# Kernel tuning notes

Hardware: AMD Instinct MI355X
Metric: run time of the kernel (lower is better)

## Reference

```python
import jax, jax.numpy as jnp
import numpy as np

NUM_SLOTS = 8
SLOT_DIM = 3
WRITE_RATE = 0.1


def _amu(x, memory, Wk, bk, Ww, bw, Wg, bg, Wo, bo):
    """Associative Memory Unit.
    x: [B, T, Din], memory: [B, N, D] -> (outputs [B, T, Dout], memory [B, N, D]).
    Per step: softmax key-addressing read, gated erase/add write at WRITE_RATE,
    output = Linear(concat(x_t, read)).
    """
    xt = jnp.swapaxes(x, 0, 1)  # [T, B, Din]

    def step(mem, x_t):
        k = x_t @ Wk + bk                                   # [B, D]
        scores = jnp.einsum('bnd,bd->bn', mem, k)           # [B, N]
        w = jax.nn.softmax(scores, axis=-1)                 # addressing weights
        read = jnp.einsum('bn,bnd->bd', w, mem)             # [B, D]
        v = x_t @ Ww + bw                                   # write vector [B, D]
        e = jax.nn.sigmoid(x_t @ Wg + bg)                   # erase gate [B, D]
        we = w[:, :, None] * e[:, None, :]                  # [B, N, D]
        mem = mem * (1.0 - WRITE_RATE * we) + WRITE_RATE * w[:, :, None] * v[:, None, :]
        out = jnp.concatenate([x_t, read], axis=-1) @ Wo + bo
        return mem, out

    mem, outs = jax.lax.scan(step, memory, xt)
    return jnp.swapaxes(outs, 0, 1), mem


def setup_inputs() -> dict:
    key = jax.random.key(0)
    ks = jax.random.split(key, 12)
    B, T, D_in, D_hid, D_out = 64, 512, 128, 512, 128
    s = 0.05
    return {
        'inp': jax.random.normal(ks[0], (B, T, D_in), jnp.float32),
        'W1k': jax.random.normal(ks[1], (D_in, SLOT_DIM), jnp.float32) * s,
        'b1k': jnp.zeros((SLOT_DIM,), jnp.float32),
        'W1w': jax.random.normal(ks[2], (D_in, SLOT_DIM), jnp.float32) * s,
        'b1w': jnp.zeros((SLOT_DIM,), jnp.float32),
        'W1g': jax.random.normal(ks[3], (D_in, SLOT_DIM), jnp.float32) * s,
        'b1g': jnp.zeros((SLOT_DIM,), jnp.float32),
        'W1o': jax.random.normal(ks[4], (D_in + SLOT_DIM, D_hid), jnp.float32) * s,
        'b1o': jnp.zeros((D_hid,), jnp.float32),
        'W2k': jax.random.normal(ks[5], (D_hid, SLOT_DIM), jnp.float32) * s,
        'b2k': jnp.zeros((SLOT_DIM,), jnp.float32),
        'W2w': jax.random.normal(ks[6], (D_hid, SLOT_DIM), jnp.float32) * s,
        'b2w': jnp.zeros((SLOT_DIM,), jnp.float32),
        'W2g': jax.random.normal(ks[7], (D_hid, SLOT_DIM), jnp.float32) * s,
        'b2g': jnp.zeros((SLOT_DIM,), jnp.float32),
        'W2o': jax.random.normal(ks[8], (D_hid + SLOT_DIM, D_out), jnp.float32) * s,
        'b2o': jnp.zeros((D_out,), jnp.float32),
    }


def reference(inp, W1k, b1k, W1w, b1w, W1g, b1g, W1o, b1o,
              W2k, b2k, W2w, b2w, W2g, b2g, W2o, b2o):
    B = inp.shape[0]
    mem0 = jnp.zeros((B, NUM_SLOTS, SLOT_DIM), inp.dtype)
    o1, mem = _amu(inp, mem0, W1k, b1k, W1w, b1w, W1g, b1g, W1o, b1o)
    o1 = jax.nn.sigmoid(o1)  # self.layers = Sequential(Sigmoid())
    o2, mem = _amu(o1, mem, W2k, b2k, W2w, b2w, W2g, b2g, W2o, b2o)
    out = jax.nn.sigmoid(o2[:, -1, :])  # last timestep, then sigmoid
    return out
```

## Files before the change

kernel.cpp:

```cpp
#include <hip/hip_runtime.h>
#include <hip/hip_bf16.h>

#define B_ 64
#define T_ 512
#define LOG2E 1.4426950408889634f
#define PHASE_STEPS 16
#define NPHASE (T_/PHASE_STEPS)

typedef __attribute__((ext_vector_type(8))) short short8;
typedef __attribute__((ext_vector_type(4))) float f32x4;

__device__ __forceinline__ float fast_exp2(float x){ return __builtin_amdgcn_exp2f(x); }
__device__ __forceinline__ float fast_rcp(float x){ return __builtin_amdgcn_rcpf(x); }
__device__ __forceinline__ float sigmoidf_(float x){ return fast_rcp(1.0f + fast_exp2(-x*LOG2E)); }
__device__ __forceinline__ unsigned short f2bf(float f){
  union{float f; unsigned u;} v; v.f = f;
  unsigned r = v.u + 0x7fffu + ((v.u>>16)&1u);
  return (unsigned short)(r>>16);
}

template<int CTRL>
__device__ __forceinline__ float dpp_xadd(float x){
  int y = __builtin_amdgcn_update_dpp(0, __float_as_int(x), CTRL, 0xf, 0xf, true);
  return x + __int_as_float(y);
}
__device__ __forceinline__ float dpp_sum8(float x){
  x = dpp_xadd<0xB1>(x);
  x = dpp_xadd<0x4E>(x);
  x = dpp_xadd<0x141>(x);
  return x;
}

__global__ __launch_bounds__(256) void k_prep(const float* __restrict__ W1o,
    const float* __restrict__ W2k, const float* __restrict__ W2w, const float* __restrict__ W2g,
    unsigned short* __restrict__ W1oTb, unsigned short* __restrict__ W2cTb)
{
  int idx = blockIdx.x*256 + threadIdx.x;
  if (idx < 65536){
    int n = idx >> 7, k = idx & 127;
    W1oTb[idx] = f2bf(W1o[k*512 + n]);
  }
  if (idx < 8192){
    int j = idx >> 9, c = idx & 511;
    float v = 0.f;
    if (j < 3) v = W2k[c*3 + j];
    else if (j < 6) v = W2w[c*3 + j - 3];
    else if (j < 9) v = W2g[c*3 + j - 6];
    W2cTb[idx] = f2bf(v);
  }
}

__global__ __launch_bounds__(256) void k_proj1(const float* __restrict__ X,
    const float* __restrict__ Wk, const float* __restrict__ bk,
    const float* __restrict__ Ww, const float* __restrict__ bw,
    const float* __restrict__ Wg, const float* __restrict__ bg,
    float* __restrict__ P1)
{
  __shared__ __align__(16) float A[64*132];
  __shared__ float Wc[128*12];
  __shared__ float bb[9];
  int tid = threadIdx.x;
  long r0 = (long)blockIdx.x * 64;
  const float4* X4 = (const float4*)(X + r0*128);
  #pragma unroll
  for (int it=0; it<8; ++it){
    int f4 = tid + it*256;
    float4 v = X4[f4];
    int f = f4*4; int row = f>>7; int k = f&127;
    A[row*132+k]   = v.x; A[row*132+k+1] = v.y;
    A[row*132+k+2] = v.z; A[row*132+k+3] = v.w;
  }
  #pragma unroll
  for (int it=0; it<5; ++it){
    int w = tid + it*256;
    if (w < 1152){
      int k = w/9, j = w%9;
      float val;
      if (j<3) val = Wk[k*3+j]; else if (j<6) val = Ww[k*3+j-3]; else val = Wg[k*3+j-6];
      Wc[k*12+j] = val;
    }
  }
  if (tid < 9){
    float v; if (tid<3) v = bk[tid]; else if (tid<6) v = bw[tid-3]; else v = bg[tid-6];
    bb[tid] = v;
  }
  __syncthreads();
  for (int o = tid; o < 576; o += 256){
    int row = o/9, j = o%9;
    float acc = bb[j];
    #pragma unroll 8
    for (int k=0;k<128;++k) acc = fmaf(A[row*132+k], Wc[k*12+j], acc);
    if (j<3) acc *= LOG2E;
    else if (j<6) acc *= 0.1f;
    else acc = 0.1f * sigmoidf_(acc);
    long r = r0 + row;
    int b = (int)(r >> 9); int t = (int)(r & 511);
    int bh = b >> 5, bl = b & 31;
    P1[((long)bh*512 + t)*288 + j*32 + bl] = acc;
  }
}

template<int STORE_ALL>
__device__ __forceinline__ void scan8(const float* __restrict__ P,
                                      float* __restrict__ Rout, int bh)
{
  __shared__ __align__(16) float buf[2][PHASE_STEPS*288];
  int tid = threadIdx.x;
  int wv = tid >> 6, lane = tid & 63;
  const float* Pb = P + (long)bh*512*288;
  if (wv == 4){
    #pragma unroll 1
    for (int p = 0; p < NPHASE; ++p){
      const float4* src = (const float4*)(Pb + (long)p*PHASE_STEPS*288);
      float4* dst = (float4*)buf[p&1];
      float4 tmp[18];
      #pragma unroll
      for (int i=0;i<18;++i) tmp[i] = src[lane + i*64];
      #pragma unroll
      for (int i=0;i<18;++i) dst[lane + i*64] = tmp[i];
      __syncthreads();
    }
  } else {
    int g = lane >> 3, slot = lane & 7;
    int bl = wv*8 + g;
    int batch = bh*32 + bl;
    float m0=0.f, m1=0.f, m2=0.f;
    __syncthreads();
    #pragma unroll 1
    for (int p = 0; p < NPHASE; ++p){
      const float* bp = buf[p&1];
      float pp[3][9];
      #pragma unroll
      for (int j=0;j<9;++j){ pp[0][j] = bp[j*32+bl]; pp[1][j] = bp[288 + j*32+bl]; }
      #pragma unroll
      for (int s=0;s<PHASE_STEPS;++s){
        if (s+2 < PHASE_STEPS){
          #pragma unroll
          for (int j=0;j<9;++j) pp[(s+2)%3][j] = bp[(s+2)*288 + j*32 + bl];
        }
        const float* pv = pp[s%3];
        float sc = fmaf(m2, pv[2], fmaf(m1, pv[1], m0*pv[0]));
        float pe = fast_exp2(sc);
        float S = dpp_sum8(pe);
        float rinv = fast_rcp(S);
        float w = pe * rinv;
        if (STORE_ALL){
          float r0 = dpp_sum8(pe*m0);
          float r1 = dpp_sum8(pe*m1);
          float r2 = dpp_sum8(pe*m2);
          float rsel = (slot==0) ? r0 : ((slot==1) ? r1 : r2);
          rsel *= rinv;
          if (slot < 3) Rout[((p*PHASE_STEPS+s)*3 + slot)*64 + batch] = rsel;
        } else if (s == PHASE_STEPS-1){
          if (p == NPHASE-1){
            float r0 = dpp_sum8(pe*m0);
            float r1 = dpp_sum8(pe*m1);
            float r2 = dpp_sum8(pe*m2);
            float rsel = (slot==0) ? r0 : ((slot==1) ? r1 : r2);
            rsel *= rinv;
            if (slot < 3) Rout[slot*64 + batch] = rsel;
          }
        }
        float v0=pv[3], v1=pv[4], v2=pv[5], e0=pv[6], e1=pv[7], e2=pv[8];
        m0 = fmaf(w, fmaf(-e0, m0, v0), m0);
        m1 = fmaf(w, fmaf(-e1, m1, v1), m1);
        m2 = fmaf(w, fmaf(-e2, m2, v2), m2);
      }
      if (p < NPHASE-1) __syncthreads();
    }
  }
}

__global__ __launch_bounds__(320) void k_scan1(const float* __restrict__ P1,
                                               float* __restrict__ R1)
{
  scan8<1>(P1, R1, (int)blockIdx.x);
}

__global__ __launch_bounds__(256) void k_fused(const float* __restrict__ X,
    const float* __restrict__ W1o, const float* __restrict__ b1o,
    const float* __restrict__ R1,
    const unsigned short* __restrict__ W1oTb, const unsigned short* __restrict__ W2cTb,
    const float* __restrict__ b2k, const float* __restrict__ b2w, const float* __restrict__ b2g,
    float* __restrict__ P2, float* __restrict__ O1last)
{
  __shared__ __align__(16) float rdS[48];
  __shared__ __align__(16) unsigned short o1b[16*520];
  __shared__ __align__(16) float pSum[4*16*16];
  int tid = threadIdx.x;
  int w = tid >> 6, lane = tid & 63;
  int n16 = lane & 15, g4 = lane >> 4;
  long r0 = (long)blockIdx.x * 16;
  int b = (int)(r0 >> 9); int t0 = (int)(r0 & 511);

  if (tid < 48){
    int i = tid/3, d = tid%3;
    rdS[tid] = R1[((t0+i)*3+d)*64 + b];
  }

  short8 afr[4];
  const float* Xrow = X + (r0 + n16)*128;
  #pragma unroll
  for (int q=0;q<4;++q){
    f32x4 x0 = *(const f32x4*)(Xrow + q*32 + g4*8);
    f32x4 x1 = *(const f32x4*)(Xrow + q*32 + g4*8 + 4);
    short8 a;
    a[0]=(short)f2bf(x0[0]); a[1]=(short)f2bf(x0[1]);
    a[2]=(short)f2bf(x0[2]); a[3]=(short)f2bf(x0[3]);
    a[4]=(short)f2bf(x1[0]); a[5]=(short)f2bf(x1[1]);
    a[6]=(short)f2bf(x1[2]); a[7]=(short)f2bf(x1[3]);
    afr[q]=a;
  }
  __syncthreads();

  f32x4 ra = *(const f32x4*)(rdS + g4*12);
  f32x4 rb = *(const f32x4*)(rdS + g4*12 + 4);
  f32x4 rc = *(const f32x4*)(rdS + g4*12 + 8);
  float rd0[4] = { ra[0], ra[3], rb[2], rc[1] };
  float rd1[4] = { ra[1], rb[0], rb[3], rc[2] };
  float rd2[4] = { ra[2], rb[1], rc[0], rc[3] };

  #pragma unroll
  for (int tt=0; tt<8; ++tt){
    int gc = w*128 + tt*16 + n16;
    f32x4 acc = {0.f,0.f,0.f,0.f};
    #pragma unroll
    for (int q=0;q<4;++q){
      short8 bf = *(const short8*)(W1oTb + gc*128 + q*32 + g4*8);
      acc = __builtin_amdgcn_mfma_f32_16x16x32_bf16(afr[q], bf, acc, 0,0,0);
    }
    float bias = b1o[gc];
    float wr0 = W1o[128*512+gc], wr1 = W1o[129*512+gc], wr2 = W1o[130*512+gc];
    #pragma unroll
    for (int reg=0; reg<4; ++reg){
      int rowloc = g4*4 + reg;
      float z = acc[reg] + bias + rd0[reg]*wr0 + rd1[reg]*wr1 + rd2[reg]*wr2;
      float o1 = sigmoidf_(z);
      o1b[rowloc*520 + gc] = f2bf(o1);
      if (t0 == 496 && rowloc == 15) O1last[b*512 + gc] = o1;
    }
  }

  f32x4 accP = {0.f,0.f,0.f,0.f};
  #pragma unroll
  for (int q2=0; q2<4; ++q2){
    int kk = w*128 + q2*32;
    short8 a2 = *(const short8*)(o1b + n16*520 + kk + g4*8);
    short8 bb2 = *(const short8*)(W2cTb + n16*512 + kk + g4*8);
    accP = __builtin_amdgcn_mfma_f32_16x16x32_bf16(a2, bb2, accP, 0,0,0);
  }
  #pragma unroll
  for (int reg=0;reg<4;++reg){
    int rowloc = g4*4+reg;
    pSum[w*256 + rowloc*16 + n16] = accP[reg];
  }
  __syncthreads();
  if (tid < 144){
    int r = tid/9, j = tid%9;
    float s = pSum[r*16+j] + pSum[256+r*16+j] + pSum[512+r*16+j] + pSum[768+r*16+j];
    float outv;
    if (j<3){ s += b2k[j]; outv = s*LOG2E; }
    else if (j<6){ s += b2w[j-3]; outv = 0.1f*s; }
    else { s += b2g[j-6]; outv = 0.1f*sigmoidf_(s); }
    int t = t0 + r;
    int bh = b >> 5, bl = b & 31;
    P2[((long)bh*512 + t)*288 + j*32 + bl] = outv;
  }
}

__global__ __launch_bounds__(320) void k_scan2_opart(const float* __restrict__ P2,
    float* __restrict__ R2F,
    const float* __restrict__ O1last, const float* __restrict__ W2o,
    const float* __restrict__ b2o, float* __restrict__ Opart)
{
  if (blockIdx.x < 2){
    scan8<0>(P2, R2F, (int)blockIdx.x);
    return;
  }
  __shared__ __align__(16) float s2[512];
  int b = blockIdx.x - 2; int tid = threadIdx.x;
  if (tid < 128)
    ((float4*)s2)[tid] = ((const float4*)(O1last + b*512))[tid];
  __syncthreads();
  if (tid < 128){
    float acc = b2o[tid];
    #pragma unroll 8
    for (int n=0;n<512;++n) acc = fmaf(s2[n], W2o[n*128+tid], acc);
    Opart[b*128+tid] = acc;
  }
}

__global__ __launch_bounds__(256) void k_final(const float* __restrict__ Opart,
    const float* __restrict__ R2F, const float* __restrict__ W2o,
    float* __restrict__ out)
{
  int idx = blockIdx.x*256 + threadIdx.x;
  if (idx < 8192){
    int b = idx >> 7; int o = idx & 127;
    float r0 = R2F[b], r1 = R2F[64+b], r2 = R2F[128+b];
    float v = Opart[idx]
            + r0*W2o[512*128+o] + r1*W2o[513*128+o] + r2*W2o[514*128+o];
    out[idx] = sigmoidf_(v);
  }
}

extern "C" void kernel_launch(void* const* d_in, const int* in_sizes, int n_in,
                              void* d_out, int out_size, void* d_ws, size_t ws_size,
                              hipStream_t stream)
{
  const float* X  = (const float*)d_in[0];
  const float* W1k= (const float*)d_in[1]; const float* b1k=(const float*)d_in[2];
  const float* W1w= (const float*)d_in[3]; const float* b1w=(const float*)d_in[4];
  const float* W1g= (const float*)d_in[5]; const float* b1g=(const float*)d_in[6];
  const float* W1o= (const float*)d_in[7]; const float* b1o=(const float*)d_in[8];
  const float* W2k= (const float*)d_in[9]; const float* b2k=(const float*)d_in[10];
  const float* W2w= (const float*)d_in[11]; const float* b2w=(const float*)d_in[12];
  const float* W2g= (const float*)d_in[13]; const float* b2g=(const float*)d_in[14];
  const float* W2o= (const float*)d_in[15]; const float* b2o=(const float*)d_in[16];

  float* ws = (float*)d_ws;
  float* P1     = ws;
  float* R1     = P1 + 294912;
  float* P2     = R1 + 98304;
  float* O1last = P2 + 294912;
  float* R2F    = O1last + 32768;
  float* Opart  = R2F + 192;
  unsigned short* W1oTb = (unsigned short*)(Opart + 8192);
  unsigned short* W2cTb = W1oTb + 65536;
  float* out    = (float*)d_out;

  hipLaunchKernelGGL(k_prep, dim3(256), dim3(256), 0, stream,
                     W1o, W2k, W2w, W2g, W1oTb, W2cTb);
  hipLaunchKernelGGL(k_proj1, dim3(512), dim3(256), 0, stream,
                     X, W1k,b1k, W1w,b1w, W1g,b1g, P1);
  hipLaunchKernelGGL(k_scan1, dim3(2), dim3(320), 0, stream, P1, R1);
  hipLaunchKernelGGL(k_fused, dim3(2048), dim3(256), 0, stream,
                     X, W1o, b1o, R1, W1oTb, W2cTb, b2k, b2w, b2g, P2, O1last);
  hipLaunchKernelGGL(k_scan2_opart, dim3(66), dim3(320), 0, stream,
                     P2, R2F, O1last, W2o, b2o, Opart);
  hipLaunchKernelGGL(k_final, dim3(32), dim3(256), 0, stream,
                     Opart, R2F, W2o, out);
}
```

Baseline: 261.7 us.

## Slim scan: per-step packed projections, drop LDS staging, defer read reduction

Projection outputs are now stored as 12-float records per (t,batch), so each scan lane loads its step's parameters straight from global memory with register prefetch. This removes the producer wave, LDS double buffering and barriers from the serial scan. Scan1 no longer reduces the read vector per step. It stores the exp weight and memory state per slot, and the fused kernel rebuilds the read vectors with DPP sums. The change also vectorises the proj1 dot products over a transposed weight tile and reuses the P1 buffer for P2. The cost is more global traffic from scan1 and the serial chain waiting on global-load latency.

New measurement: 430.4 us. 64.4% more time.

```diff
diff --git a/kernel.cpp b/kernel.cpp
--- a/kernel.cpp
+++ b/kernel.cpp
@@ -4,8 +4,6 @@
 #define B_ 64
 #define T_ 512
 #define LOG2E 1.4426950408889634f
-#define PHASE_STEPS 16
-#define NPHASE (T_/PHASE_STEPS)
 
 typedef __attribute__((ext_vector_type(8))) short short8;
 typedef __attribute__((ext_vector_type(4))) float f32x4;
@@ -57,7 +55,7 @@
     float* __restrict__ P1)
 {
   __shared__ __align__(16) float A[64*132];
-  __shared__ float Wc[128*12];
+  __shared__ __align__(16) float WcT[9*132];
   __shared__ float bb[9];
   int tid = threadIdx.x;
   long r0 = (long)blockIdx.x * 64;
@@ -67,17 +65,16 @@
     int f4 = tid + it*256;
     float4 v = X4[f4];
     int f = f4*4; int row = f>>7; int k = f&127;
-    A[row*132+k]   = v.x; A[row*132+k+1] = v.y;
-    A[row*132+k+2] = v.z; A[row*132+k+3] = v.w;
+    *(float4*)&A[row*132+k] = v;
   }
   #pragma unroll
   for (int it=0; it<5; ++it){
-    int w = tid + it*256;
-    if (w < 1152){
-      int k = w/9, j = w%9;
+    int w0 = tid + it*256;
+    if (w0 < 1152){
+      int k = w0/9, j = w0%9;
       float val;
       if (j<3) val = Wk[k*3+j]; else if (j<6) val = Ww[k*3+j-3]; else val = Wg[k*3+j-6];
-      Wc[k*12+j] = val;
+      WcT[j*132+k] = val;
     }
   }
   if (tid < 9){
@@ -87,99 +84,88 @@
   __syncthreads();
   for (int o = tid; o < 576; o += 256){
     int row = o/9, j = o%9;
-    float acc = bb[j];
-    #pragma unroll 8
-    for (int k=0;k<128;++k) acc = fmaf(A[row*132+k], Wc[k*12+j], acc);
+    const f32x4* Ar = (const f32x4*)(A + row*132);
+    const f32x4* Wr = (const f32x4*)(WcT + j*132);
+    f32x4 acc4 = {0.f,0.f,0.f,0.f};
+    #pragma unroll
+    for (int k4=0;k4<32;++k4){
+      f32x4 a = Ar[k4], wv = Wr[k4];
+      acc4[0]=fmaf(a[0],wv[0],acc4[0]);
+      acc4[1]=fmaf(a[1],wv[1],acc4[1]);
+      acc4[2]=fmaf(a[2],wv[2],acc4[2]);
+      acc4[3]=fmaf(a[3],wv[3],acc4[3]);
+    }
+    float acc = bb[j] + (acc4[0]+acc4[1]) + (acc4[2]+acc4[3]);
     if (j<3) acc *= LOG2E;
     else if (j<6) acc *= 0.1f;
     else acc = 0.1f * sigmoidf_(acc);
     long r = r0 + row;
     int b = (int)(r >> 9); int t = (int)(r & 511);
-    int bh = b >> 5, bl = b & 31;
-    P1[((long)bh*512 + t)*288 + j*32 + bl] = acc;
-  }
-}
-
-template<int STORE_ALL>
-__device__ __forceinline__ void scan8(const float* __restrict__ P,
-                                      float* __restrict__ Rout, int bh)
-{
-  __shared__ __align__(16) float buf[2][PHASE_STEPS*288];
+    P1[((long)t*64 + b)*12 + j] = acc;
+  }
+}
+
+template<int STORE_SM>
+__device__ __forceinline__ void scan_slim(const float* __restrict__ P,
+                                          float* __restrict__ Out, int bh)
+{
   int tid = threadIdx.x;
-  int wv = tid >> 6, lane = tid & 63;
-  const float* Pb = P + (long)bh*512*288;
-  if (wv == 4){
-    #pragma unroll 1
-    for (int p = 0; p < NPHASE; ++p){
-      const float4* src = (const float4*)(Pb + (long)p*PHASE_STEPS*288);
-      float4* dst = (float4*)buf[p&1];
-      float4 tmp[18];
-      #pragma unroll
-      for (int i=0;i<18;++i) tmp[i] = src[lane + i*64];
-      #pragma unroll
-      for (int i=0;i<18;++i) dst[lane + i*64] = tmp[i];
-      __syncthreads();
-    }
-  } else {
-    int g = lane >> 3, slot = lane & 7;
-    int bl = wv*8 + g;
-    int batch = bh*32 + bl;
-    float m0=0.f, m1=0.f, m2=0.f;
-    __syncthreads();
-    #pragma unroll 1
-    for (int p = 0; p < NPHASE; ++p){
-      const float* bp = buf[p&1];
-      float pp[3][9];
-      #pragma unroll
-      for (int j=0;j<9;++j){ pp[0][j] = bp[j*32+bl]; pp[1][j] = bp[288 + j*32+bl]; }
-      #pragma unroll
-      for (int s=0;s<PHASE_STEPS;++s){
-        if (s+2 < PHASE_STEPS){
-          #pragma unroll
-          for (int j=0;j<9;++j) pp[(s+2)%3][j] = bp[(s+2)*288 + j*32 + bl];
-        }
-        const float* pv = pp[s%3];
-        float sc = fmaf(m2, pv[2], fmaf(m1, pv[1], m0*pv[0]));
-        float pe = fast_exp2(sc);
-        float S = dpp_sum8(pe);
-        float rinv = fast_rcp(S);
-        float w = pe * rinv;
-        if (STORE_ALL){
-          float r0 = dpp_sum8(pe*m0);
-          float r1 = dpp_sum8(pe*m1);
-          float r2 = dpp_sum8(pe*m2);
-          float rsel = (slot==0) ? r0 : ((slot==1) ? r1 : r2);
-          rsel *= rinv;
-          if (slot < 3) Rout[((p*PHASE_STEPS+s)*3 + slot)*64 + batch] = rsel;
-        } else if (s == PHASE_STEPS-1){
-          if (p == NPHASE-1){
-            float r0 = dpp_sum8(pe*m0);
-            float r1 = dpp_sum8(pe*m1);
-            float r2 = dpp_sum8(pe*m2);
-            float rsel = (slot==0) ? r0 : ((slot==1) ? r1 : r2);
-            rsel *= rinv;
-            if (slot < 3) Rout[slot*64 + batch] = rsel;
-          }
-        }
-        float v0=pv[3], v1=pv[4], v2=pv[5], e0=pv[6], e1=pv[7], e2=pv[8];
-        m0 = fmaf(w, fmaf(-e0, m0, v0), m0);
-        m1 = fmaf(w, fmaf(-e1, m1, v1), m1);
-        m2 = fmaf(w, fmaf(-e2, m2, v2), m2);
+  int lane = tid & 63, wv = tid >> 6;
+  if (lane >= 32) return;
+  int g = lane >> 3, slot = lane & 7;
+  int batch = bh*32 + wv*4 + g;
+  const f32x4* Pp = (const f32x4*)P + batch*3;
+  float* So = Out + ((long)batch*8 + slot)*4;
+
+  f32x4 pf[4][3];
+  #pragma unroll
+  for (int u=0; u<4; ++u){
+    pf[u][0] = Pp[u*192+0]; pf[u][1] = Pp[u*192+1]; pf[u][2] = Pp[u*192+2];
+  }
+  float m0=0.f, m1=0.f, m2=0.f;
+
+  #pragma unroll 1
+  for (int tb=0; tb<512; tb+=4){
+    #pragma unroll
+    for (int u=0; u<4; ++u){
+      int t = tb + u;
+      f32x4 A0=pf[u][0], A1=pf[u][1], A2=pf[u][2];
+      if (t+4 < 512){
+        pf[u][0]=Pp[(t+4)*192]; pf[u][1]=Pp[(t+4)*192+1]; pf[u][2]=Pp[(t+4)*192+2];
       }
-      if (p < NPHASE-1) __syncthreads();
-    }
-  }
-}
-
-__global__ __launch_bounds__(320) void k_scan1(const float* __restrict__ P1,
-                                               float* __restrict__ R1)
-{
-  scan8<1>(P1, R1, (int)blockIdx.x);
+      float sc = fmaf(m2, A0[2], fmaf(m1, A0[1], m0*A0[0]));
+      float pe = fast_exp2(sc);
+      float S = dpp_sum8(pe);
+      float rinv = fast_rcp(S);
+      float w = pe * rinv;
+      if (STORE_SM){
+        f32x4 sv; sv[0]=pe; sv[1]=m0; sv[2]=m1; sv[3]=m2;
+        *(f32x4*)(So + (long)t*2048) = sv;
+      } else if (t == 511){
+        float r0 = dpp_sum8(pe*m0);
+        float r1 = dpp_sum8(pe*m1);
+        float r2 = dpp_sum8(pe*m2);
+        float rsel = (slot==0) ? r0 : ((slot==1) ? r1 : r2);
+        rsel *= rinv;
+        if (slot < 3) Out[slot*64 + batch] = rsel;
+      }
+      float v0=A0[3], v1=A1[0], v2=A1[1], e0=A1[2], e1=A1[3], e2=A2[0];
+      m0 = fmaf(w, fmaf(-e0, m0, v0), m0);
+      m1 = fmaf(w, fmaf(-e1, m1, v1), m1);
+      m2 = fmaf(w, fmaf(-e2, m2, v2), m2);
+    }
+  }
+}
+
+__global__ __launch_bounds__(512) void k_scan1(const float* __restrict__ P1,
+                                               float* __restrict__ SM)
+{
+  scan_slim<1>(P1, SM, (int)blockIdx.x);
 }
 
 __global__ __launch_bounds__(256) void k_fused(const float* __restrict__ X,
     const float* __restrict__ W1o, const float* __restrict__ b1o,
-    const float* __restrict__ R1,
+    const float* __restrict__ SM,
     const unsigned short* __restrict__ W1oTb, const unsigned short* __restrict__ W2cTb,
     const float* __restrict__ b2k, const float* __restrict__ b2w, const float* __restrict__ b2g,
     float* __restrict__ P2, float* __restrict__ O1last)
@@ -193,9 +179,16 @@
   long r0 = (long)blockIdx.x * 16;
   int b = (int)(r0 >> 9); int t0 = (int)(r0 & 511);
 
-  if (tid < 48){
-    int i = tid/3, d = tid%3;
-    rdS[tid] = R1[((t0+i)*3+d)*64 + b];
+  if (tid < 128){
+    int i = tid >> 3, slot = tid & 7;
+    f32x4 v = *(const f32x4*)(SM + (((long)(t0+i)*64 + b)*8 + slot)*4);
+    float S   = dpp_sum8(v[0]);
+    float r0v = dpp_sum8(v[0]*v[1]);
+    float r1v = dpp_sum8(v[0]*v[2]);
+    float r2v = dpp_sum8(v[0]*v[3]);
+    float rinv = fast_rcp(S);
+    float rsel = (slot==0) ? r0v : ((slot==1) ? r1v : r2v);
+    if (slot < 3) rdS[i*3+slot] = rsel*rinv;
   }
 
   short8 afr[4];
@@ -263,18 +256,17 @@
     else if (j<6){ s += b2w[j-3]; outv = 0.1f*s; }
     else { s += b2g[j-6]; outv = 0.1f*sigmoidf_(s); }
     int t = t0 + r;
-    int bh = b >> 5, bl = b & 31;
-    P2[((long)bh*512 + t)*288 + j*32 + bl] = outv;
-  }
-}
-
-__global__ __launch_bounds__(320) void k_scan2_opart(const float* __restrict__ P2,
+    P2[((long)t*64 + b)*12 + j] = outv;
+  }
+}
+
+__global__ __launch_bounds__(512) void k_scan2_opart(const float* __restrict__ P2,
     float* __restrict__ R2F,
     const float* __restrict__ O1last, const float* __restrict__ W2o,
     const float* __restrict__ b2o, float* __restrict__ Opart)
 {
   if (blockIdx.x < 2){
-    scan8<0>(P2, R2F, (int)blockIdx.x);
+    scan_slim<0>(P2, R2F, (int)blockIdx.x);
     return;
   }
   __shared__ __align__(16) float s2[512];
@@ -320,23 +312,23 @@
 
   float* ws = (float*)d_ws;
   float* P1     = ws;
-  float* R1     = P1 + 294912;
-  float* P2     = R1 + 98304;
-  float* O1last = P2 + 294912;
+  float* SM     = P1 + 393216;
+  float* O1last = SM + 1048576;
   float* R2F    = O1last + 32768;
   float* Opart  = R2F + 192;
   unsigned short* W1oTb = (unsigned short*)(Opart + 8192);
   unsigned short* W2cTb = W1oTb + 65536;
+  float* P2     = P1;
   float* out    = (float*)d_out;
 
   hipLaunchKernelGGL(k_prep, dim3(256), dim3(256), 0, stream,
                      W1o, W2k, W2w, W2g, W1oTb, W2cTb);
   hipLaunchKernelGGL(k_proj1, dim3(512), dim3(256), 0, stream,
                      X, W1k,b1k, W1w,b1w, W1g,b1g, P1);
-  hipLaunchKernelGGL(k_scan1, dim3(2), dim3(320), 0, stream, P1, R1);
+  hipLaunchKernelGGL(k_scan1, dim3(2), dim3(512), 0, stream, P1, SM);
   hipLaunchKernelGGL(k_fused, dim3(2048), dim3(256), 0, stream,
-                     X, W1o, b1o, R1, W1oTb, W2cTb, b2k, b2w, b2g, P2, O1last);
-  hipLaunchKernelGGL(k_scan2_opart, dim3(66), dim3(320), 0, stream,
+                     X, W1o, b1o, SM, W1oTb, W2cTb, b2k, b2w, b2g, P2, O1last);
+  hipLaunchKernelGGL(k_scan2_opart, dim3(66), dim3(512), 0, stream,
                      P2, R2F, O1last, W2o, b2o, Opart);
   hipLaunchKernelGGL(k_final, dim3(32), dim3(256), 0, stream,
                      Opart, R2F, W2o, out);
```
